# Performance work log

Measured on AMD Instinct MI355X. Metric: run time of the kernel, lower is better.

Reference implementation:

```python
import jax, jax.numpy as jnp
import numpy as np

HEADS, HD = 8, 64

def swish(x):
    return x * jax.nn.sigmoid(x)

def layer_norm(x, eps=1e-5):
    mu = jnp.mean(x, axis=-1, keepdims=True)
    var = jnp.var(x, axis=-1, keepdims=True)
    return (x - mu) / jnp.sqrt(var + eps)

def setup_inputs() -> dict:
    key = jax.random.key(0)
    k1, k2, k3 = jax.random.split(key, 3)
    B, L, D = 2, 2048, 512
    x = jax.random.normal(k1, (B, L, D), jnp.float32)
    cnn_w = jax.random.normal(k2, (HEADS * HD * 3, D, 3), jnp.float32) * 0.02
    cnn_b = jnp.zeros((HEADS * HD * 3,), jnp.float32)
    fc_w = jax.random.normal(k3, (D, HEADS * HD), jnp.float32) * 0.02
    fc_b = jnp.zeros((D,), jnp.float32)
    return {"x": x, "cnn_w": cnn_w, "cnn_b": cnn_b, "fc_w": fc_w, "fc_b": fc_b}

def reference(x, cnn_w, cnn_b, fc_w, fc_b):
    B, L, D = x.shape
    # Conv1d(dims -> heads*hd*3, kernel=3, stride=1, pad=1) on channel-first layout
    xt = jnp.transpose(x, (0, 2, 1))  # [B, D, L]
    y = jax.lax.conv_general_dilated(
        xt, cnn_w, window_strides=(1,), padding=[(1, 1)],
        dimension_numbers=("NCH", "OIH", "NCH"),
    ) + cnn_b[None, :, None]  # [B, 3*H*HD, L]
    qkv = swish(y).reshape(B, HEADS, HD * 3, L)
    q, k, v = jnp.split(qkv, 3, axis=-2)  # each [B, H, HD, L]
    # NOTE: original scales by sqrt(length), not sqrt(hd)
    scores = jnp.einsum("bhdw,bhdm->bhwm", q, k) / jnp.sqrt(jnp.float32(L))
    att = jax.nn.softmax(scores, axis=-1)  # [B, H, L, L]
    new_v = jnp.einsum("bhwm,bhdm->bwhd", att, v).reshape(B, L, HEADS * HD)
    m = swish(new_v @ fc_w.T + fc_b)  # [B, L, D]
    return layer_norm(x * 2 + m)
```

## Files before the change

### kernel.cpp

```cpp
#include <hip/hip_runtime.h>
#include <hip/hip_bf16.h>

#define BB 2
#define LL 2048
#define DD 512
#define HH 8
#define HDM 64
#define SCALE 0.022097086912079608f
#define QSCALE 0.03187935766f

typedef __hip_bfloat16 bf16;
typedef unsigned short u16;
typedef __attribute__((ext_vector_type(8))) short short8v;
typedef __attribute__((ext_vector_type(4))) float float4v;

#define XN  2097152
#define WN  2359296
#define BN  1536
#define FWN 262144
#define FBN 512

__device__ __forceinline__ float b2f(u16 u) {
    return __uint_as_float(((unsigned int)u) << 16);
}
__device__ __forceinline__ u16 f2u(float f) {
    bf16 h = __float2bfloat16(f);
    u16 r;
    __builtin_memcpy(&r, &h, 2);
    return r;
}
__device__ __forceinline__ void unpack8(uint4 p, float* f) {
    f[0] = __uint_as_float(p.x << 16); f[1] = __uint_as_float(p.x & 0xffff0000u);
    f[2] = __uint_as_float(p.y << 16); f[3] = __uint_as_float(p.y & 0xffff0000u);
    f[4] = __uint_as_float(p.z << 16); f[5] = __uint_as_float(p.z & 0xffff0000u);
    f[6] = __uint_as_float(p.w << 16); f[7] = __uint_as_float(p.w & 0xffff0000u);
}
__device__ __forceinline__ uint4 pack8(const float* f) {
    uint4 p;
    p.x = (unsigned)f2u(f[0]) | ((unsigned)f2u(f[1]) << 16);
    p.y = (unsigned)f2u(f[2]) | ((unsigned)f2u(f[3]) << 16);
    p.z = (unsigned)f2u(f[4]) | ((unsigned)f2u(f[5]) << 16);
    p.w = (unsigned)f2u(f[6]) | ((unsigned)f2u(f[7]) << 16);
    return p;
}

__device__ __forceinline__ void gld_lds16(const u16* g, u16* l) {
    __builtin_amdgcn_global_load_lds(
        (const __attribute__((address_space(1))) unsigned int*)g,
        (__attribute__((address_space(3))) unsigned int*)l, 16, 0, 0);
}

__global__ void detect_kernel(const u16* __restrict__ x, int* __restrict__ flag) {
    int bad = 0;
    for (int i = threadIdx.x; i < 256; i += 64) {
        float v = b2f(x[i]);
        if (!(fabsf(v) < 100.f)) bad = 1;
    }
    unsigned long long m = __ballot(bad);
    if (threadIdx.x == 0) *flag = (m != 0ull) ? 1 : 0;
}

__global__ __launch_bounds__(256) void convert_kernel(
    const void* __restrict__ src, u16* __restrict__ dst, int n,
    const int* __restrict__ flagp)
{
    const int flag = *flagp;
    int i = (blockIdx.x * 256 + threadIdx.x) * 8;
    if (i >= n) return;
    if (flag) {
        const float* s = (const float*)src;
        float f[8];
        float4 a = *(const float4*)(s + i);
        float4 b = *(const float4*)(s + i + 4);
        f[0] = a.x; f[1] = a.y; f[2] = a.z; f[3] = a.w;
        f[4] = b.x; f[5] = b.y; f[6] = b.z; f[7] = b.w;
        *(uint4*)(dst + i) = pack8(f);
    } else {
        *(uint4*)(dst + i) = *(const uint4*)((const u16*)src + i);
    }
}

__global__ __launch_bounds__(256) void convert_xpad_kernel(
    const void* __restrict__ src, u16* __restrict__ xp,
    const int* __restrict__ flagp)
{
    const int flag = *flagp;
    int idx = blockIdx.x * 256 + threadIdx.x;
    if (idx < 256) {
        int b2  = idx >> 7;
        int r2  = (idx >> 6) & 1;
        int c82 = (idx & 63) * 8;
        size_t off = ((size_t)(b2 * 2050 + (r2 ? 2049 : 0))) * 512 + c82;
        uint4 z = {0u, 0u, 0u, 0u};
        *(uint4*)(xp + off) = z;
    }
    if (idx >= BB * LL * 64) return;
    int b   = idx / (LL * 64);
    int rem = idx - b * (LL * 64);
    int l   = rem >> 6;
    int c8  = (rem & 63) * 8;
    size_t si = ((size_t)(b * LL + l)) * 512 + c8;
    size_t di = ((size_t)(b * 2050 + l + 1)) * 512 + c8;
    if (flag) {
        const float* s = (const float*)src;
        float f[8];
        float4 a = *(const float4*)(s + si);
        float4 bq = *(const float4*)(s + si + 4);
        f[0] = a.x; f[1] = a.y; f[2] = a.z; f[3] = a.w;
        f[4] = bq.x; f[5] = bq.y; f[6] = bq.z; f[7] = bq.w;
        *(uint4*)(xp + di) = pack8(f);
    } else {
        *(uint4*)(xp + di) = *(const uint4*)((const u16*)src + si);
    }
}

__global__ __launch_bounds__(256) void convw_kernel(
    const void* __restrict__ src, u16* __restrict__ wt,
    const int* __restrict__ flagp)
{
    const int flag = *flagp;
    int idx = blockIdx.x * 256 + threadIdx.x;
    int i8  = idx & 63;
    int rem = idx >> 6;
    int k   = rem % 3;
    int o   = rem / 3;
    float f[8];
    if (flag) {
        const float* s = (const float*)src;
#pragma unroll
        for (int j = 0; j < 8; ++j) f[j] = s[(size_t)o * 1536 + (i8 * 8 + j) * 3 + k];
    } else {
        const u16* s = (const u16*)src;
#pragma unroll
        for (int j = 0; j < 8; ++j) f[j] = b2f(s[(size_t)o * 1536 + (i8 * 8 + j) * 3 + k]);
    }
    *(uint4*)(wt + (size_t)o * 1536 + k * 512 + i8 * 8) = pack8(f);
}

__global__ __launch_bounds__(256) void conv_mfma_kernel(
    const u16* __restrict__ xp,
    const u16* __restrict__ wt,
    const u16* __restrict__ bias,
    u16* __restrict__ qkbuf,
    u16* __restrict__ vbuf)
{
    __shared__ u16 smem[32768];
    u16* Asb = smem;
    u16* Bsb = smem + 2 * 128 * 64;
#define OTS 140
    u16* OT  = smem;

    const int blk = blockIdx.x;
    const int rt = blk / 12;
    const int ct = blk - rt * 12;
    const int b  = rt >> 4;
    const int l0 = (rt & 15) * 128;
    const int tid  = threadIdx.x;
    const int wave = tid >> 6;
    const int lane = tid & 63;
    const int quad = lane >> 4;
    const int l16  = lane & 15;
    const int e7   = l16 & 7;
    const int wx = wave & 1;
    const int wy = wave >> 1;

    float4v acc[4][4];
#pragma unroll
    for (int mt = 0; mt < 4; ++mt)
#pragma unroll
        for (int nt = 0; nt < 4; ++nt) acc[mt][nt] = (float4v){0.f, 0.f, 0.f, 0.f};

    const int rowW = wave * 32;
    const int lrow = lane >> 3;
    const int g8   = (((lane & 7) ^ lrow)) * 8;
    auto stage = [&](int kc, int buf) {
        const int slab = kc >> 3;
        const int i0   = (kc & 7) * 64;
        const u16* ga = xp + ((size_t)(b * 2050 + l0 + rowW + slab + lrow)) * 512 + i0 + g8;
        const u16* gb = wt + ((size_t)(ct * 128 + rowW + lrow)) * 1536 + kc * 64 + g8;
        u16* la = Asb + (size_t)(buf * 128 + rowW) * 64;
        u16* lb = Bsb + (size_t)(buf * 128 + rowW) * 64;
#pragma unroll
        for (int j = 0; j < 4; ++j) {
            gld_lds16(ga + (size_t)(j * 8) * 512,  la + (j * 8) * 64);
            gld_lds16(gb + (size_t)(j * 8) * 1536, lb + (j * 8) * 64);
        }
    };

    stage(0, 0);

    for (int kc = 0; kc < 24; ++kc) {
        const int cur = kc & 1;
        __syncthreads();

        if (kc < 23) stage(kc + 1, 1 - cur);

#pragma unroll
        for (int half = 0; half < 2; ++half) {
            const int p = ((half * 4 + quad) ^ e7) * 8;
            short8v aF[4], bF[4];
#pragma unroll
            for (int mt = 0; mt < 4; ++mt)
                aF[mt] = *(const short8v*)&Asb[(size_t)(cur * 128 + wy * 64 + mt * 16 + l16) * 64 + p];
#pragma unroll
            for (int nt = 0; nt < 4; ++nt)
                bF[nt] = *(const short8v*)&Bsb[(size_t)(cur * 128 + wx * 64 + nt * 16 + l16) * 64 + p];
#pragma unroll
            for (int mt = 0; mt < 4; ++mt)
#pragma unroll
                for (int nt = 0; nt < 4; ++nt)
                    acc[mt][nt] = __builtin_amdgcn_mfma_f32_16x16x32_bf16(
                        aF[mt], bF[nt], acc[mt][nt], 0, 0, 0);
        }
    }

    __syncthreads();
    {
        const int tloc = (ct * 2 + wx) % 3;
#pragma unroll
        for (int nt = 0; nt < 4; ++nt) {
            int oc = wx * 64 + nt * 16 + l16;
            float bb = b2f(bias[ct * 128 + oc]);
#pragma unroll
            for (int mt = 0; mt < 4; ++mt)
#pragma unroll
                for (int r = 0; r < 4; ++r) {
                    int lr = wy * 64 + mt * 16 + quad * 4 + r;
                    float y = acc[mt][nt][r] + bb;
                    y = y / (1.f + __expf(-y));
                    if (tloc == 0) y *= QSCALE;
                    OT[lr * OTS + oc] = f2u(y);
                }
        }
    }
    __syncthreads();

#pragma unroll
    for (int g = 0; g < 2; ++g) {
        int a  = ct * 2 + g;
        int t  = a % 3;
        int bh = b * HH + a / 3;
        if (t != 2) {
            u16* base = qkbuf + ((size_t)((bh * 2 + t) * LL + l0)) * HDM;
#pragma unroll
            for (int it = 0; it < 4; ++it) {
                int idx = it * 256 + tid;
                int l   = idx >> 3;
                int d8  = (idx & 7) * 8;
                uint4 val = *(const uint4*)&OT[l * OTS + g * 64 + d8];
                *(uint4*)(base + (size_t)l * HDM + d8) = val;
            }
        } else {
            u16* base = vbuf + ((size_t)(bh * HDM)) * LL + l0;
#pragma unroll
            for (int it = 0; it < 4; ++it) {
                int idx = it * 256 + tid;
                int dd  = idx >> 4;
                int l8  = (idx & 15) * 8;
                u16 tmp[8];
#pragma unroll
                for (int j = 0; j < 8; ++j) tmp[j] = OT[(l8 + j) * OTS + g * 64 + dd];
                uint4 val;
                val.x = (unsigned)tmp[0] | ((unsigned)tmp[1] << 16);
                val.y = (unsigned)tmp[2] | ((unsigned)tmp[3] << 16);
                val.z = (unsigned)tmp[4] | ((unsigned)tmp[5] << 16);
                val.w = (unsigned)tmp[6] | ((unsigned)tmp[7] << 16);
                *(uint4*)(base + (size_t)dd * LL + l8) = val;
            }
        }
    }
#undef OTS
}

__global__ __launch_bounds__(256) void attn_mfma_kernel(
    const u16* __restrict__ qk,
    const u16* __restrict__ v,
    u16* __restrict__ newv)
{
    __shared__ u16 kts[2][64][64];
    __shared__ u16 vts[2][64][64];
    __shared__ u16 pts[4][16][76];

    const int blkid = blockIdx.x;
    const int bh = blkid >> 5;
    const int wc = blkid & 31;
    const int b  = bh >> 3;
    const int h  = bh & 7;
    const int tid  = threadIdx.x;
    const int wave = tid >> 6;
    const int lane = tid & 63;
    const int quad = lane >> 4;
    const int l16  = lane & 15;
    const int e7   = l16 & 7;

    const u16* qbase = qk + ((size_t)(bh * 2 + 0)) * LL * HDM;
    const u16* kbase = qk + ((size_t)(bh * 2 + 1)) * LL * HDM;
    const u16* vbase = v + (size_t)bh * HDM * LL;

    const int w0 = wc * 64 + wave * 16;

    short8v qfrag[2];
    qfrag[0] = *(const short8v*)(qbase + (size_t)(w0 + l16) * HDM + quad * 8);
    qfrag[1] = *(const short8v*)(qbase + (size_t)(w0 + l16) * HDM + 32 + quad * 8);

    short8v vones;
    {
        short o1 = (l16 == 0) ? (short)0x3F80 : (short)0;
#pragma unroll
        for (int j = 0; j < 8; ++j) vones[j] = o1;
    }

    float4v oacc[4];
#pragma unroll
    for (int dt = 0; dt < 4; ++dt) oacc[dt] = (float4v){0.f, 0.f, 0.f, 0.f};
    float4v lacc = (float4v){0.f, 0.f, 0.f, 0.f};

    const int rbase = wave * 16;
    const int lrow  = lane >> 3;
    const int g8    = ((lane & 7) ^ lrow) * 8;
    auto stage = [&](int ic, int buf) {
        const int m0 = ic * 64;
#pragma unroll
        for (int j = 0; j < 2; ++j) {
            gld_lds16(kbase + (size_t)(m0 + rbase + j * 8 + lrow) * HDM + g8,
                      &kts[buf][rbase + j * 8][0]);
            gld_lds16(vbase + (size_t)(rbase + j * 8 + lrow) * LL + m0 + g8,
                      &vts[buf][rbase + j * 8][0]);
        }
    };

    stage(0, 0);

    for (int ic = 0; ic < 32; ++ic) {
        const int cur = ic & 1;
        __syncthreads();

        if (ic < 31) stage(ic + 1, 1 - cur);

        const int p0 = (quad ^ e7) * 8;
        const int p1 = ((quad + 4) ^ e7) * 8;

        float4v s[4];
#pragma unroll
        for (int mt = 0; mt < 4; ++mt) {
            s[mt] = (float4v){0.f, 0.f, 0.f, 0.f};
            short8v b0 = *(const short8v*)&kts[cur][mt * 16 + l16][p0];
            s[mt] = __builtin_amdgcn_mfma_f32_16x16x32_bf16(qfrag[0], b0, s[mt], 0, 0, 0);
            short8v b1 = *(const short8v*)&kts[cur][mt * 16 + l16][p1];
            s[mt] = __builtin_amdgcn_mfma_f32_16x16x32_bf16(qfrag[1], b1, s[mt], 0, 0, 0);
        }

#pragma unroll
        for (int mt = 0; mt < 4; ++mt)
#pragma unroll
            for (int r = 0; r < 4; ++r)
                pts[wave][quad * 4 + r][mt * 16 + l16] =
                    f2u(__builtin_amdgcn_exp2f(s[mt][r]));

        short8v pa0 = *(const short8v*)&pts[wave][l16][quad * 8];
        short8v pa1 = *(const short8v*)&pts[wave][l16][32 + quad * 8];

        lacc = __builtin_amdgcn_mfma_f32_16x16x32_bf16(pa0, vones, lacc, 0, 0, 0);
        lacc = __builtin_amdgcn_mfma_f32_16x16x32_bf16(pa1, vones, lacc, 0, 0, 0);

#pragma unroll
        for (int dt = 0; dt < 4; ++dt) {
            short8v v0 = *(const short8v*)&vts[cur][dt * 16 + l16][p0];
            oacc[dt] = __builtin_amdgcn_mfma_f32_16x16x32_bf16(pa0, v0, oacc[dt], 0, 0, 0);
            short8v v1 = *(const short8v*)&vts[cur][dt * 16 + l16][p1];
            oacc[dt] = __builtin_amdgcn_mfma_f32_16x16x32_bf16(pa1, v1, oacc[dt], 0, 0, 0);
        }
    }

    float inv[4];
#pragma unroll
    for (int r = 0; r < 4; ++r) {
        float lsum = __shfl(lacc[r], quad * 16);
        inv[r] = 1.f / lsum;
    }
    u16* ob = newv + (size_t)b * LL * 512 + h * 64;
#pragma unroll
    for (int dt = 0; dt < 4; ++dt)
#pragma unroll
        for (int r = 0; r < 4; ++r) {
            int w = w0 + quad * 4 + r;
            ob[(size_t)w * 512 + dt * 16 + l16] = f2u(oacc[dt][r] * inv[r]);
        }
}

__global__ __launch_bounds__(256) void fc_ln_mfma_kernel(
    const u16* __restrict__ newv,
    const u16* __restrict__ fcw,
    const u16* __restrict__ fcb,
    const u16* __restrict__ xp,
    void* __restrict__ out,
    const int* __restrict__ flagp)
{
    const int l0 = blockIdx.x * 16;
    const int tid  = threadIdx.x;
    const int wave = tid >> 6;
    const int lane = tid & 63;
    const int quad = lane >> 4;
    const int l16  = lane & 15;
    const int col0 = wave * 128;

    const int bb_ = l0 >> 11;
    const size_t xbase = ((size_t)(bb_ * 2050 + (l0 & 2047) + 1)) * 512;

    __shared__ float psum[4][16], psq[4][16];

    short8v aF[16];
    const u16* arow = newv + (size_t)(l0 + l16) * 512 + quad * 8;
#pragma unroll
    for (int kc = 0; kc < 16; ++kc)
        aF[kc] = *(const short8v*)(arow + kc * 32);

    float4v acc[8];
#pragma unroll
    for (int nt = 0; nt < 8; ++nt) acc[nt] = (float4v){0.f, 0.f, 0.f, 0.f};

#pragma unroll
    for (int nt = 0; nt < 8; ++nt) {
        const u16* brow = fcw + (size_t)(col0 + nt * 16 + l16) * 512 + quad * 8;
#pragma unroll
        for (int kc = 0; kc < 16; ++kc) {
            short8v bF = *(const short8v*)(brow + kc * 32);
            acc[nt] = __builtin_amdgcn_mfma_f32_16x16x32_bf16(aF[kc], bF, acc[nt], 0, 0, 0);
        }
    }

    float z[8][4];
    float rs[4] = {0.f, 0.f, 0.f, 0.f}, rq[4] = {0.f, 0.f, 0.f, 0.f};
#pragma unroll
    for (int nt = 0; nt < 8; ++nt) {
        int col = col0 + nt * 16 + l16;
        float bb = b2f(fcb[col]);
#pragma unroll
        for (int r = 0; r < 4; ++r) {
            int row = quad * 4 + r;
            float y = acc[nt][r] + bb;
            float sw = y / (1.f + __expf(-y));
            float xv = b2f(xp[xbase + (size_t)row * 512 + col]);
            float zz = xv * 2.f + sw;
            z[nt][r] = zz;
            rs[r] += zz;
            rq[r] += zz * zz;
        }
    }
#pragma unroll
    for (int msk = 1; msk <= 8; msk <<= 1)
#pragma unroll
        for (int r = 0; r < 4; ++r) {
            rs[r] += __shfl_xor(rs[r], msk);
            rq[r] += __shfl_xor(rq[r], msk);
        }
    if (l16 == 0) {
#pragma unroll
        for (int r = 0; r < 4; ++r) {
            psum[wave][quad * 4 + r] = rs[r];
            psq[wave][quad * 4 + r]  = rq[r];
        }
    }
    __syncthreads();

    float mu[4], inv[4];
#pragma unroll
    for (int r = 0; r < 4; ++r) {
        int row = quad * 4 + r;
        float s = psum[0][row] + psum[1][row] + psum[2][row] + psum[3][row];
        float q = psq[0][row] + psq[1][row] + psq[2][row] + psq[3][row];
        float m = s * (1.f / 512.f);
        float var = q * (1.f / 512.f) - m * m;
        mu[r] = m;
        inv[r] = rsqrtf(var + 1e-5f);
    }

    const int flag = *flagp;
#pragma unroll
    for (int nt = 0; nt < 8; ++nt) {
        int col = col0 + nt * 16 + l16;
#pragma unroll
        for (int r = 0; r < 4; ++r) {
            int row = quad * 4 + r;
            float val = (z[nt][r] - mu[r]) * inv[r];
            if (flag) ((float*)out)[(size_t)(l0 + row) * 512 + col] = val;
            else      ((u16*)out)[(size_t)(l0 + row) * 512 + col] = f2u(val);
        }
    }
}

extern "C" void kernel_launch(void* const* d_in, const int* in_sizes, int n_in,
                              void* d_out, int out_size, void* d_ws, size_t ws_size,
                              hipStream_t stream) {
    (void)in_sizes; (void)n_in; (void)out_size; (void)ws_size;

    char* ws = (char*)d_ws;
    int* flag = (int*)ws;
    u16* xp   = (u16*)(ws + 256);
    u16* wtc  = (u16*)(ws + 4198656);
    u16* bc   = (u16*)(ws + 8917248);
    u16* fwc  = (u16*)(ws + 8920320);
    u16* fbc  = (u16*)(ws + 9444608);
    u16* qkb  = (u16*)(ws + 9445632);
    u16* vb   = (u16*)(ws + 17834240);
    u16* nvc  = (u16*)(ws + 22028544);

    detect_kernel<<<dim3(1), dim3(64), 0, stream>>>((const u16*)d_in[0], flag);

    convert_xpad_kernel<<<dim3((BB * LL * 64 + 255) / 256), dim3(256), 0, stream>>>(d_in[0], xp, flag);
    convw_kernel<<<dim3(1152), dim3(256), 0, stream>>>(d_in[1], wtc, flag);
    convert_kernel<<<dim3((BN + 2047) / 2048), dim3(256), 0, stream>>>(d_in[2], bc,  BN,  flag);
    convert_kernel<<<dim3((FWN + 2047) / 2048), dim3(256), 0, stream>>>(d_in[3], fwc, FWN, flag);
    convert_kernel<<<dim3((FBN + 2047) / 2048), dim3(256), 0, stream>>>(d_in[4], fbc, FBN, flag);

    conv_mfma_kernel<<<dim3(32 * 12), dim3(256), 0, stream>>>(xp, wtc, bc, qkb, vb);
    attn_mfma_kernel<<<dim3(BB * HH * (LL / 64)), dim3(256), 0, stream>>>(qkb, vb, nvc);
    fc_ln_mfma_kernel<<<dim3(256), dim3(256), 0, stream>>>(nvc, fwc, fbc, xp, d_out, flag);
}
```

Baseline: 180.2 us.

## Double attention key-chunk to 128 and merge small conversion launches

```diff
diff --git a/kernel.cpp b/kernel.cpp
--- a/kernel.cpp
+++ b/kernel.cpp
@@ -29,12 +29,6 @@
     __builtin_memcpy(&r, &h, 2);
     return r;
 }
-__device__ __forceinline__ void unpack8(uint4 p, float* f) {
-    f[0] = __uint_as_float(p.x << 16); f[1] = __uint_as_float(p.x & 0xffff0000u);
-    f[2] = __uint_as_float(p.y << 16); f[3] = __uint_as_float(p.y & 0xffff0000u);
-    f[4] = __uint_as_float(p.z << 16); f[5] = __uint_as_float(p.z & 0xffff0000u);
-    f[6] = __uint_as_float(p.w << 16); f[7] = __uint_as_float(p.w & 0xffff0000u);
-}
 __device__ __forceinline__ uint4 pack8(const float* f) {
     uint4 p;
     p.x = (unsigned)f2u(f[0]) | ((unsigned)f2u(f[1]) << 16);
@@ -60,13 +54,7 @@
     if (threadIdx.x == 0) *flag = (m != 0ull) ? 1 : 0;
 }
 
-__global__ __launch_bounds__(256) void convert_kernel(
-    const void* __restrict__ src, u16* __restrict__ dst, int n,
-    const int* __restrict__ flagp)
-{
-    const int flag = *flagp;
-    int i = (blockIdx.x * 256 + threadIdx.x) * 8;
-    if (i >= n) return;
+__device__ __forceinline__ void conv8(const void* src, u16* dst, size_t i, int flag) {
     if (flag) {
         const float* s = (const float*)src;
         float f[8];
@@ -77,6 +65,23 @@
         *(uint4*)(dst + i) = pack8(f);
     } else {
         *(uint4*)(dst + i) = *(const uint4*)((const u16*)src + i);
+    }
+}
+
+__global__ __launch_bounds__(256) void convert_small_kernel(
+    const void* __restrict__ bsrc, const void* __restrict__ fwsrc,
+    const void* __restrict__ fbsrc,
+    u16* __restrict__ bc, u16* __restrict__ fwc, u16* __restrict__ fbc,
+    const int* __restrict__ flagp)
+{
+    const int flag = *flagp;
+    int o = blockIdx.x * 256 + threadIdx.x;
+    if (o < BN / 8) {
+        conv8(bsrc, bc, (size_t)o * 8, flag);
+    } else if (o < BN / 8 + FWN / 8) {
+        conv8(fwsrc, fwc, (size_t)(o - BN / 8) * 8, flag);
+    } else if (o < BN / 8 + FWN / 8 + FBN / 8) {
+        conv8(fbsrc, fbc, (size_t)(o - BN / 8 - FWN / 8) * 8, flag);
     }
 }
 
@@ -277,8 +282,8 @@
     const u16* __restrict__ v,
     u16* __restrict__ newv)
 {
-    __shared__ u16 kts[2][64][64];
-    __shared__ u16 vts[2][64][64];
+    __shared__ u16 kts[2][128][64];
+    __shared__ u16 vts[2][64][128];
     __shared__ u16 pts[4][16][76];
 
     const int blkid = blockIdx.x;
@@ -315,60 +320,63 @@
     for (int dt = 0; dt < 4; ++dt) oacc[dt] = (float4v){0.f, 0.f, 0.f, 0.f};
     float4v lacc = (float4v){0.f, 0.f, 0.f, 0.f};
 
-    const int rbase = wave * 16;
-    const int lrow  = lane >> 3;
-    const int g8    = ((lane & 7) ^ lrow) * 8;
+    const int rbK   = wave * 32;
+    const int lrowK = lane >> 3;
+    const int gK    = ((lane & 7) ^ lrowK) * 8;
+    const int rbV   = wave * 16;
+    const int lrowV = lane >> 4;
     auto stage = [&](int ic, int buf) {
-        const int m0 = ic * 64;
-#pragma unroll
-        for (int j = 0; j < 2; ++j) {
-            gld_lds16(kbase + (size_t)(m0 + rbase + j * 8 + lrow) * HDM + g8,
-                      &kts[buf][rbase + j * 8][0]);
-            gld_lds16(vbase + (size_t)(rbase + j * 8 + lrow) * LL + m0 + g8,
-                      &vts[buf][rbase + j * 8][0]);
+        const int m0 = ic * 128;
+#pragma unroll
+        for (int j = 0; j < 4; ++j) {
+            gld_lds16(kbase + (size_t)(m0 + rbK + j * 8 + lrowK) * HDM + gK,
+                      &kts[buf][rbK + j * 8][0]);
+            const int vrow = j * 4 + lrowV;
+            gld_lds16(vbase + (size_t)(rbV + vrow) * LL + m0 + (((lane & 15) ^ vrow) * 8),
+                      &vts[buf][rbV + j * 4][0]);
         }
     };
 
     stage(0, 0);
 
-    for (int ic = 0; ic < 32; ++ic) {
+    for (int ic = 0; ic < 16; ++ic) {
         const int cur = ic & 1;
         __syncthreads();
 
-        if (ic < 31) stage(ic + 1, 1 - cur);
-
-        const int p0 = (quad ^ e7) * 8;
-        const int p1 = ((quad + 4) ^ e7) * 8;
-
-        float4v s[4];
-#pragma unroll
-        for (int mt = 0; mt < 4; ++mt) {
+        if (ic < 15) stage(ic + 1, 1 - cur);
+
+        float4v s[8];
+#pragma unroll
+        for (int mt = 0; mt < 8; ++mt) {
             s[mt] = (float4v){0.f, 0.f, 0.f, 0.f};
-            short8v b0 = *(const short8v*)&kts[cur][mt * 16 + l16][p0];
+            short8v b0 = *(const short8v*)&kts[cur][mt * 16 + l16][((quad) ^ e7) * 8];
             s[mt] = __builtin_amdgcn_mfma_f32_16x16x32_bf16(qfrag[0], b0, s[mt], 0, 0, 0);
-            short8v b1 = *(const short8v*)&kts[cur][mt * 16 + l16][p1];
+            short8v b1 = *(const short8v*)&kts[cur][mt * 16 + l16][((quad + 4) ^ e7) * 8];
             s[mt] = __builtin_amdgcn_mfma_f32_16x16x32_bf16(qfrag[1], b1, s[mt], 0, 0, 0);
         }
 
 #pragma unroll
-        for (int mt = 0; mt < 4; ++mt)
-#pragma unroll
-            for (int r = 0; r < 4; ++r)
-                pts[wave][quad * 4 + r][mt * 16 + l16] =
-                    f2u(__builtin_amdgcn_exp2f(s[mt][r]));
-
-        short8v pa0 = *(const short8v*)&pts[wave][l16][quad * 8];
-        short8v pa1 = *(const short8v*)&pts[wave][l16][32 + quad * 8];
-
-        lacc = __builtin_amdgcn_mfma_f32_16x16x32_bf16(pa0, vones, lacc, 0, 0, 0);
-        lacc = __builtin_amdgcn_mfma_f32_16x16x32_bf16(pa1, vones, lacc, 0, 0, 0);
-
-#pragma unroll
-        for (int dt = 0; dt < 4; ++dt) {
-            short8v v0 = *(const short8v*)&vts[cur][dt * 16 + l16][p0];
-            oacc[dt] = __builtin_amdgcn_mfma_f32_16x16x32_bf16(pa0, v0, oacc[dt], 0, 0, 0);
-            short8v v1 = *(const short8v*)&vts[cur][dt * 16 + l16][p1];
-            oacc[dt] = __builtin_amdgcn_mfma_f32_16x16x32_bf16(pa1, v1, oacc[dt], 0, 0, 0);
+        for (int g = 0; g < 2; ++g) {
+#pragma unroll
+            for (int mt4 = 0; mt4 < 4; ++mt4)
+#pragma unroll
+                for (int r = 0; r < 4; ++r)
+                    pts[wave][quad * 4 + r][mt4 * 16 + l16] =
+                        f2u(__builtin_amdgcn_exp2f(s[g * 4 + mt4][r]));
+
+            short8v pa0 = *(const short8v*)&pts[wave][l16][quad * 8];
+            short8v pa1 = *(const short8v*)&pts[wave][l16][32 + quad * 8];
+
+            lacc = __builtin_amdgcn_mfma_f32_16x16x32_bf16(pa0, vones, lacc, 0, 0, 0);
+            lacc = __builtin_amdgcn_mfma_f32_16x16x32_bf16(pa1, vones, lacc, 0, 0, 0);
+
+#pragma unroll
+            for (int dt = 0; dt < 4; ++dt) {
+                short8v v0 = *(const short8v*)&vts[cur][dt * 16 + l16][((g * 8 + quad) ^ l16) * 8];
+                oacc[dt] = __builtin_amdgcn_mfma_f32_16x16x32_bf16(pa0, v0, oacc[dt], 0, 0, 0);
+                short8v v1 = *(const short8v*)&vts[cur][dt * 16 + l16][((g * 8 + 4 + quad) ^ l16) * 8];
+                oacc[dt] = __builtin_amdgcn_mfma_f32_16x16x32_bf16(pa1, v1, oacc[dt], 0, 0, 0);
+            }
         }
     }
 
@@ -509,9 +517,8 @@
 
     convert_xpad_kernel<<<dim3((BB * LL * 64 + 255) / 256), dim3(256), 0, stream>>>(d_in[0], xp, flag);
     convw_kernel<<<dim3(1152), dim3(256), 0, stream>>>(d_in[1], wtc, flag);
-    convert_kernel<<<dim3((BN + 2047) / 2048), dim3(256), 0, stream>>>(d_in[2], bc,  BN,  flag);
-    convert_kernel<<<dim3((FWN + 2047) / 2048), dim3(256), 0, stream>>>(d_in[3], fwc, FWN, flag);
-    convert_kernel<<<dim3((FBN + 2047) / 2048), dim3(256), 0, stream>>>(d_in[4], fbc, FBN, flag);
+    convert_small_kernel<<<dim3((BN / 8 + FWN / 8 + FBN / 8 + 255) / 256), dim3(256), 0, stream>>>(
+        d_in[2], d_in[3], d_in[4], bc, fwc, fbc, flag);
 
     conv_mfma_kernel<<<dim3(32 * 12), dim3(256), 0, stream>>>(xp, wtc, bc, qkb, vb);
     attn_mfma_kernel<<<dim3(BB * HH * (LL / 64)), dim3(256), 0, stream>>>(qkb, vb, nvc);
```

Result: faster. 171.6 us (-4.7%).

## Software-pipeline PV matmul one step behind QK in attention, merge small converts

Applied to the files above, without the earlier changes.

```diff
diff --git a/kernel.cpp b/kernel.cpp
--- a/kernel.cpp
+++ b/kernel.cpp
@@ -29,12 +29,6 @@
     __builtin_memcpy(&r, &h, 2);
     return r;
 }
-__device__ __forceinline__ void unpack8(uint4 p, float* f) {
-    f[0] = __uint_as_float(p.x << 16); f[1] = __uint_as_float(p.x & 0xffff0000u);
-    f[2] = __uint_as_float(p.y << 16); f[3] = __uint_as_float(p.y & 0xffff0000u);
-    f[4] = __uint_as_float(p.z << 16); f[5] = __uint_as_float(p.z & 0xffff0000u);
-    f[6] = __uint_as_float(p.w << 16); f[7] = __uint_as_float(p.w & 0xffff0000u);
-}
 __device__ __forceinline__ uint4 pack8(const float* f) {
     uint4 p;
     p.x = (unsigned)f2u(f[0]) | ((unsigned)f2u(f[1]) << 16);
@@ -60,13 +54,7 @@
     if (threadIdx.x == 0) *flag = (m != 0ull) ? 1 : 0;
 }
 
-__global__ __launch_bounds__(256) void convert_kernel(
-    const void* __restrict__ src, u16* __restrict__ dst, int n,
-    const int* __restrict__ flagp)
-{
-    const int flag = *flagp;
-    int i = (blockIdx.x * 256 + threadIdx.x) * 8;
-    if (i >= n) return;
+__device__ __forceinline__ void conv8(const void* src, u16* dst, size_t i, int flag) {
     if (flag) {
         const float* s = (const float*)src;
         float f[8];
@@ -77,6 +65,23 @@
         *(uint4*)(dst + i) = pack8(f);
     } else {
         *(uint4*)(dst + i) = *(const uint4*)((const u16*)src + i);
+    }
+}
+
+__global__ __launch_bounds__(256) void convert_small_kernel(
+    const void* __restrict__ bsrc, const void* __restrict__ fwsrc,
+    const void* __restrict__ fbsrc,
+    u16* __restrict__ bc, u16* __restrict__ fwc, u16* __restrict__ fbc,
+    const int* __restrict__ flagp)
+{
+    const int flag = *flagp;
+    int o = blockIdx.x * 256 + threadIdx.x;
+    if (o < BN / 8) {
+        conv8(bsrc, bc, (size_t)o * 8, flag);
+    } else if (o < BN / 8 + FWN / 8) {
+        conv8(fwsrc, fwc, (size_t)(o - BN / 8) * 8, flag);
+    } else if (o < BN / 8 + FWN / 8 + FBN / 8) {
+        conv8(fbsrc, fbc, (size_t)(o - BN / 8 - FWN / 8) * 8, flag);
     }
 }
 
@@ -278,7 +283,7 @@
     u16* __restrict__ newv)
 {
     __shared__ u16 kts[2][64][64];
-    __shared__ u16 vts[2][64][64];
+    __shared__ u16 vts[3][64][64];
     __shared__ u16 pts[4][16][76];
 
     const int blkid = blockIdx.x;
@@ -318,36 +323,51 @@
     const int rbase = wave * 16;
     const int lrow  = lane >> 3;
     const int g8    = ((lane & 7) ^ lrow) * 8;
-    auto stage = [&](int ic, int buf) {
+    auto stage = [&](int ic, int kb, int vb2) {
         const int m0 = ic * 64;
 #pragma unroll
         for (int j = 0; j < 2; ++j) {
             gld_lds16(kbase + (size_t)(m0 + rbase + j * 8 + lrow) * HDM + g8,
-                      &kts[buf][rbase + j * 8][0]);
+                      &kts[kb][rbase + j * 8][0]);
             gld_lds16(vbase + (size_t)(rbase + j * 8 + lrow) * LL + m0 + g8,
-                      &vts[buf][rbase + j * 8][0]);
+                      &vts[vb2][rbase + j * 8][0]);
         }
     };
 
-    stage(0, 0);
+    stage(0, 0, 0);
+
+    const int p0 = (quad ^ e7) * 8;
+    const int p1 = ((quad + 4) ^ e7) * 8;
+
+    short8v pa0o, pa1o;
 
     for (int ic = 0; ic < 32; ++ic) {
-        const int cur = ic & 1;
+        const int ck = ic & 1;
         __syncthreads();
 
-        if (ic < 31) stage(ic + 1, 1 - cur);
-
-        const int p0 = (quad ^ e7) * 8;
-        const int p1 = ((quad + 4) ^ e7) * 8;
+        if (ic < 31) stage(ic + 1, 1 - ck, (ic + 1) % 3);
 
         float4v s[4];
 #pragma unroll
         for (int mt = 0; mt < 4; ++mt) {
             s[mt] = (float4v){0.f, 0.f, 0.f, 0.f};
-            short8v b0 = *(const short8v*)&kts[cur][mt * 16 + l16][p0];
+            short8v b0 = *(const short8v*)&kts[ck][mt * 16 + l16][p0];
             s[mt] = __builtin_amdgcn_mfma_f32_16x16x32_bf16(qfrag[0], b0, s[mt], 0, 0, 0);
-            short8v b1 = *(const short8v*)&kts[cur][mt * 16 + l16][p1];
+            short8v b1 = *(const short8v*)&kts[ck][mt * 16 + l16][p1];
             s[mt] = __builtin_amdgcn_mfma_f32_16x16x32_bf16(qfrag[1], b1, s[mt], 0, 0, 0);
+        }
+
+        if (ic > 0) {
+            const int pv = (ic - 1) % 3;
+            lacc = __builtin_amdgcn_mfma_f32_16x16x32_bf16(pa0o, vones, lacc, 0, 0, 0);
+            lacc = __builtin_amdgcn_mfma_f32_16x16x32_bf16(pa1o, vones, lacc, 0, 0, 0);
+#pragma unroll
+            for (int dt = 0; dt < 4; ++dt) {
+                short8v v0 = *(const short8v*)&vts[pv][dt * 16 + l16][p0];
+                oacc[dt] = __builtin_amdgcn_mfma_f32_16x16x32_bf16(pa0o, v0, oacc[dt], 0, 0, 0);
+                short8v v1 = *(const short8v*)&vts[pv][dt * 16 + l16][p1];
+                oacc[dt] = __builtin_amdgcn_mfma_f32_16x16x32_bf16(pa1o, v1, oacc[dt], 0, 0, 0);
+            }
         }
 
 #pragma unroll
@@ -357,18 +377,20 @@
                 pts[wave][quad * 4 + r][mt * 16 + l16] =
                     f2u(__builtin_amdgcn_exp2f(s[mt][r]));
 
-        short8v pa0 = *(const short8v*)&pts[wave][l16][quad * 8];
-        short8v pa1 = *(const short8v*)&pts[wave][l16][32 + quad * 8];
-
-        lacc = __builtin_amdgcn_mfma_f32_16x16x32_bf16(pa0, vones, lacc, 0, 0, 0);
-        lacc = __builtin_amdgcn_mfma_f32_16x16x32_bf16(pa1, vones, lacc, 0, 0, 0);
-
+        pa0o = *(const short8v*)&pts[wave][l16][quad * 8];
+        pa1o = *(const short8v*)&pts[wave][l16][32 + quad * 8];
+    }
+
+    {
+        const int pv = 31 % 3;
+        lacc = __builtin_amdgcn_mfma_f32_16x16x32_bf16(pa0o, vones, lacc, 0, 0, 0);
+        lacc = __builtin_amdgcn_mfma_f32_16x16x32_bf16(pa1o, vones, lacc, 0, 0, 0);
 #pragma unroll
         for (int dt = 0; dt < 4; ++dt) {
-            short8v v0 = *(const short8v*)&vts[cur][dt * 16 + l16][p0];
-            oacc[dt] = __builtin_amdgcn_mfma_f32_16x16x32_bf16(pa0, v0, oacc[dt], 0, 0, 0);
-            short8v v1 = *(const short8v*)&vts[cur][dt * 16 + l16][p1];
-            oacc[dt] = __builtin_amdgcn_mfma_f32_16x16x32_bf16(pa1, v1, oacc[dt], 0, 0, 0);
+            short8v v0 = *(const short8v*)&vts[pv][dt * 16 + l16][p0];
+            oacc[dt] = __builtin_amdgcn_mfma_f32_16x16x32_bf16(pa0o, v0, oacc[dt], 0, 0, 0);
+            short8v v1 = *(const short8v*)&vts[pv][dt * 16 + l16][p1];
+            oacc[dt] = __builtin_amdgcn_mfma_f32_16x16x32_bf16(pa1o, v1, oacc[dt], 0, 0, 0);
         }
     }
 
@@ -509,9 +531,8 @@
 
     convert_xpad_kernel<<<dim3((BB * LL * 64 + 255) / 256), dim3(256), 0, stream>>>(d_in[0], xp, flag);
     convw_kernel<<<dim3(1152), dim3(256), 0, stream>>>(d_in[1], wtc, flag);
-    convert_kernel<<<dim3((BN + 2047) / 2048), dim3(256), 0, stream>>>(d_in[2], bc,  BN,  flag);
-    convert_kernel<<<dim3((FWN + 2047) / 2048), dim3(256), 0, stream>>>(d_in[3], fwc, FWN, flag);
-    convert_kernel<<<dim3((FBN + 2047) / 2048), dim3(256), 0, stream>>>(d_in[4], fbc, FBN, flag);
+    convert_small_kernel<<<dim3((BN / 8 + FWN / 8 + FBN / 8 + 255) / 256), dim3(256), 0, stream>>>(
+        d_in[2], d_in[3], d_in[4], bc, fwc, fbc, flag);
 
     conv_mfma_kernel<<<dim3(32 * 12), dim3(256), 0, stream>>>(xp, wtc, bc, qkb, vb);
     attn_mfma_kernel<<<dim3(BB * HH * (LL / 64)), dim3(256), 0, stream>>>(qkb, vb, nvc);
```

Result: no change. 180.4 us (+0.1%).
